# Performance work log

Hardware: AMD Instinct MI355X
Metric: run time of the kernel (lower is better)

## Reference

```python
import jax, jax.numpy as jnp
import numpy as np

PAD = 1
STRIDE = 1


def setup_inputs() -> dict:
    key = jax.random.key(0)
    kx, kw, kb = jax.random.split(key, 3)
    C_IN, C_OUT, K, H, W = 128, 256, 3, 256, 256
    lim = 1.0 / np.sqrt(C_IN * K * K)
    x = jax.random.normal(kx, (C_IN, H, W), dtype=jnp.float32)
    weight = jax.random.uniform(kw, (C_OUT, C_IN, K, K), minval=-lim, maxval=lim, dtype=jnp.float32)
    bias = jax.random.uniform(kb, (C_OUT, 1, 1), minval=-lim, maxval=lim, dtype=jnp.float32)
    return {"x": x, "weight": weight, "bias": bias}


def reference(x, weight, bias):
    # Original does per-channel jnp.pad then a scan-based im2col + einsum
    # 'oijk,ihwjk->ohw'. That is exactly a standard cross-correlation conv,
    # expressed here with the efficient fused primitive (same math).
    out = jax.lax.conv_general_dilated(
        x[None],                      # (1, c, h, w)
        weight,                       # (o, i, k, k)
        window_strides=(STRIDE, STRIDE),
        padding=[(PAD, PAD), (PAD, PAD)],
        dimension_numbers=("NCHW", "OIHW", "NCHW"),
    )[0]                              # (o, h', w')
    return out + bias
```

## Files before the change

### kernel.cpp

```cpp
#include <hip/hip_runtime.h>
#include <hip/hip_bf16.h>
#include <stdint.h>


#define CIN   128
#define COUT  256
#define HH    256
#define WW    256
#define HP    258
#define WP    258
#define XP_ELEMS (HP * WP * CIN)

typedef __attribute__((ext_vector_type(8))) __bf16 bf16x8;
typedef __attribute__((ext_vector_type(4))) float  floatx4;
typedef __attribute__((ext_vector_type(8))) short  short8;

__global__ void zero_border(unsigned short* __restrict__ xp) {
    int p  = blockIdx.x;
    int ch = threadIdx.x;
    int hp, wp;
    if (p < 258)      { hp = 0;   wp = p; }
    else if (p < 516) { hp = 257; wp = p - 258; }
    else { int s = p - 516; hp = 1 + (s >> 1); wp = (s & 1) * 257; }
    xp[(hp * WP + wp) * CIN + ch] = 0;
}

__global__ __launch_bounds__(256) void xpose_pad(const float* __restrict__ x,
                                                 unsigned short* __restrict__ xp) {
    __shared__ __align__(16) unsigned short tile[64][136];
    int h  = blockIdx.x;
    int w0 = blockIdx.y << 6;
    int t  = threadIdx.x;
    int wl  = t & 63;
    int icq = t >> 6;
    const float* src = x + h * WW + w0 + wl;
#pragma unroll
    for (int icb = 0; icb < 32; ++icb) {
        int ic = icb * 4 + icq;
        __hip_bfloat16 b = __float2bfloat16(src[ic * (HH * WW)]);
        tile[wl][ic] = __builtin_bit_cast(unsigned short, b);
    }
    __syncthreads();
    int wl2 = t >> 2, q = t & 3;
    const short8* s8 = (const short8*)&tile[wl2][q * 32];
    short8* d8 = (short8*)(xp + ((size_t)(h + 1) * WP + (w0 + 1) + wl2) * CIN + q * 32);
#pragma unroll
    for (int i = 0; i < 4; ++i) d8[i] = s8[i];
}

__global__ __launch_bounds__(256) void wpack(const float* __restrict__ w,
                                             unsigned short* __restrict__ wp) {
    int idx = blockIdx.x * 256 + threadIdx.x;
    int kk  = idx >> 15;
    int rem = idx & 32767;
    __hip_bfloat16 b = __float2bfloat16(w[rem * 9 + kk]);
    wp[idx] = __builtin_bit_cast(unsigned short, b);
}

__global__ __launch_bounds__(512, 2) void conv_mfma(
    const unsigned short* __restrict__ xp,
    const unsigned short* __restrict__ wpk,
    const float* __restrict__ bias,
    float* __restrict__ out) {
    __shared__ __align__(16) unsigned short x_lds[2 * 16384];

    const int tid  = threadIdx.x;
    const int lane = tid & 63;
    const int wv   = tid >> 6;
    const int l15  = lane & 15;
    const int lg   = lane >> 4;
    const int wave_m = (wv >> 2) << 7;
    const int wave_n = (wv & 3) << 6;

    const int orig = blockIdx.x;
    const int h    = ((orig & 7) << 5) | (orig >> 3);

    const int s0 = (tid & 255) * CIN + (tid >> 8) * 8;

    auto stage = [&](int buf, int kh, int kw, int kk, int icq) {
        unsigned short* base = x_lds + buf * 16384;
        const unsigned short* asrc = wpk + (size_t)kk * (COUT * CIN) + icq * 32 + s0;
        const unsigned short* bsrc = xp + ((size_t)(h + kh) * WP + kw) * CIN + icq * 32 + s0;
        __builtin_amdgcn_global_load_lds(
            (const __attribute__((address_space(1))) void*)asrc,
            (__attribute__((address_space(3))) void*)(base + tid * 8), 16, 0, 0);
        __builtin_amdgcn_global_load_lds(
            (const __attribute__((address_space(1))) void*)(asrc + 16),
            (__attribute__((address_space(3))) void*)(base + 4096 + tid * 8), 16, 0, 0);
        __builtin_amdgcn_global_load_lds(
            (const __attribute__((address_space(1))) void*)bsrc,
            (__attribute__((address_space(3))) void*)(base + 8192 + tid * 8), 16, 0, 0);
        __builtin_amdgcn_global_load_lds(
            (const __attribute__((address_space(1))) void*)(bsrc + 16),
            (__attribute__((address_space(3))) void*)(base + 12288 + tid * 8), 16, 0, 0);
    };

    floatx4 acc[8][4];
#pragma unroll
    for (int fi = 0; fi < 8; ++fi)
#pragma unroll
        for (int fj = 0; fj < 4; ++fj) {
            floatx4 z = {0.f, 0.f, 0.f, 0.f};
            acc[fi][fj] = z;
        }

    stage(0, 0, 0, 0, 0);
    __syncthreads();

#pragma unroll
    for (int kk = 0; kk < 9; ++kk) {
#pragma unroll
        for (int icq = 0; icq < 4; ++icq) {
            const int t   = kk * 4 + icq;
            const int cur = t & 1;

            if (t < 35) {
                const int tn  = t + 1;
                const int kkn = tn >> 2, icqn = tn & 3;
                const int khn = kkn / 3, kwn = kkn - khn * 3;
                stage(cur ^ 1, khn, kwn, kkn, icqn);
            }

            const unsigned short* Ab = x_lds + cur * 16384;
            const unsigned short* Bb = Ab + 8192;
            bf16x8 a[8], b[4];
#pragma unroll
            for (int fj = 0; fj < 4; ++fj)
                b[fj] = *(const bf16x8*)(Bb + (lg * 256 + wave_n + fj * 16 + l15) * 8);
#pragma unroll
            for (int fi = 0; fi < 8; ++fi)
                a[fi] = *(const bf16x8*)(Ab + (lg * 256 + wave_m + fi * 16 + l15) * 8);

            __builtin_amdgcn_s_setprio(1);
#pragma unroll
            for (int fi = 0; fi < 8; ++fi)
#pragma unroll
                for (int fj = 0; fj < 4; ++fj)
                    acc[fi][fj] = __builtin_amdgcn_mfma_f32_16x16x32_bf16(
                        a[fi], b[fj], acc[fi][fj], 0, 0, 0);
            __builtin_amdgcn_s_setprio(0);

            __syncthreads();
        }
    }

    const int nbase = h * WW + wave_n + l15;
#pragma unroll
    for (int fi = 0; fi < 8; ++fi) {
        int mrow = wave_m + fi * 16 + lg * 4;
#pragma unroll
        for (int r = 0; r < 4; ++r) {
            float bv = bias[mrow + r];
#pragma unroll
            for (int fj = 0; fj < 4; ++fj)
                out[(size_t)(mrow + r) * (HH * WW) + nbase + fj * 16] = acc[fi][fj][r] + bv;
        }
    }
}

extern "C" void kernel_launch(void* const* d_in, const int* in_sizes, int n_in,
                              void* d_out, int out_size, void* d_ws, size_t ws_size,
                              hipStream_t stream) {
    (void)in_sizes; (void)n_in; (void)out_size; (void)ws_size;
    const float* x    = (const float*)d_in[0];
    const float* w    = (const float*)d_in[1];
    const float* bias = (const float*)d_in[2];
    float* out = (float*)d_out;

    unsigned short* xp  = (unsigned short*)d_ws;
    unsigned short* wpk = xp + XP_ELEMS;

    zero_border<<<dim3(1028), dim3(128), 0, stream>>>(xp);
    xpose_pad<<<dim3(256, 4), dim3(256), 0, stream>>>(x, xp);
    wpack<<<dim3(1152), dim3(256), 0, stream>>>(w, wpk);
    conv_mfma<<<dim3(256), dim3(512), 0, stream>>>(xp, wpk, bias, out);
}
```

Before: 154.8 us.

## Merge prep kernels and double K-chunk per stage with XOR-swizzled LDS

Three preprocessing kernels (border zeroing, transpose-pad, weight pack) are merged into one launch, and the border zeroing now uses 16-byte stores. The conv kernel stages 64 input channels per step instead of 32, halving the number of barriers (18 stages instead of 36), and stores rows of 64 contiguous channels with an XOR swizzle to avoid LDS bank conflicts. LDS use doubles to 128 KB per block, which at two blocks per CU may exceed LDS capacity and reduce occupancy.

```diff
diff --git a/kernel.cpp b/kernel.cpp
--- a/kernel.cpp
+++ b/kernel.cpp
@@ -15,46 +15,51 @@
 typedef __attribute__((ext_vector_type(4))) float  floatx4;
 typedef __attribute__((ext_vector_type(8))) short  short8;
 
-__global__ void zero_border(unsigned short* __restrict__ xp) {
-    int p  = blockIdx.x;
-    int ch = threadIdx.x;
-    int hp, wp;
-    if (p < 258)      { hp = 0;   wp = p; }
-    else if (p < 516) { hp = 257; wp = p - 258; }
-    else { int s = p - 516; hp = 1 + (s >> 1); wp = (s & 1) * 257; }
-    xp[(hp * WP + wp) * CIN + ch] = 0;
-}
+#define AS1 __attribute__((address_space(1)))
+#define AS3 __attribute__((address_space(3)))
 
-__global__ __launch_bounds__(256) void xpose_pad(const float* __restrict__ x,
-                                                 unsigned short* __restrict__ xp) {
+__global__ __launch_bounds__(256) void prep(const float* __restrict__ x,
+                                            const float* __restrict__ w,
+                                            unsigned short* __restrict__ xp,
+                                            unsigned short* __restrict__ wpk) {
     __shared__ __align__(16) unsigned short tile[64][136];
-    int h  = blockIdx.x;
-    int w0 = blockIdx.y << 6;
-    int t  = threadIdx.x;
-    int wl  = t & 63;
-    int icq = t >> 6;
-    const float* src = x + h * WW + w0 + wl;
+    const int bid = blockIdx.x;
+    const int t   = threadIdx.x;
+    if (bid < 1024) {
+        int h  = bid >> 2;
+        int w0 = (bid & 3) << 6;
+        int wl = t & 63, icq = t >> 6;
+        const float* src = x + h * WW + w0 + wl;
 #pragma unroll
-    for (int icb = 0; icb < 32; ++icb) {
-        int ic = icb * 4 + icq;
-        __hip_bfloat16 b = __float2bfloat16(src[ic * (HH * WW)]);
-        tile[wl][ic] = __builtin_bit_cast(unsigned short, b);
+        for (int icb = 0; icb < 32; ++icb) {
+            int ic = icb * 4 + icq;
+            __hip_bfloat16 b = __float2bfloat16(src[ic * (HH * WW)]);
+            tile[wl][ic] = __builtin_bit_cast(unsigned short, b);
+        }
+        __syncthreads();
+        int wl2 = t >> 2, q = t & 3;
+        const short8* s8 = (const short8*)&tile[wl2][q * 32];
+        short8* d8 = (short8*)(xp + ((size_t)(h + 1) * WP + (w0 + 1) + wl2) * CIN + q * 32);
+#pragma unroll
+        for (int i = 0; i < 4; ++i) d8[i] = s8[i];
+    } else if (bid < 2176) {
+        int idx = (bid - 1024) * 256 + t;
+        int kk  = idx >> 15;
+        int rem = idx & 32767;
+        __hip_bfloat16 b = __float2bfloat16(w[rem * 9 + kk]);
+        wpk[idx] = __builtin_bit_cast(unsigned short, b);
+    } else {
+        int cid = (bid - 2176) * 256 + t;
+        if (cid < 16448) {
+            int p = cid >> 4, oct = cid & 15;
+            int hp, wp;
+            if (p < 258)      { hp = 0;   wp = p; }
+            else if (p < 516) { hp = 257; wp = p - 258; }
+            else { int s = p - 516; hp = 1 + (s >> 1); wp = (s & 1) * 257; }
+            short8 z = {0, 0, 0, 0, 0, 0, 0, 0};
+            *(short8*)(xp + ((size_t)hp * WP + wp) * CIN + oct * 8) = z;
+        }
     }
-    __syncthreads();
-    int wl2 = t >> 2, q = t & 3;
-    const short8* s8 = (const short8*)&tile[wl2][q * 32];
-    short8* d8 = (short8*)(xp + ((size_t)(h + 1) * WP + (w0 + 1) + wl2) * CIN + q * 32);
-#pragma unroll
-    for (int i = 0; i < 4; ++i) d8[i] = s8[i];
-}
-
-__global__ __launch_bounds__(256) void wpack(const float* __restrict__ w,
-                                             unsigned short* __restrict__ wp) {
-    int idx = blockIdx.x * 256 + threadIdx.x;
-    int kk  = idx >> 15;
-    int rem = idx & 32767;
-    __hip_bfloat16 b = __float2bfloat16(w[rem * 9 + kk]);
-    wp[idx] = __builtin_bit_cast(unsigned short, b);
 }
 
 __global__ __launch_bounds__(512, 2) void conv_mfma(
@@ -62,7 +67,7 @@
     const unsigned short* __restrict__ wpk,
     const float* __restrict__ bias,
     float* __restrict__ out) {
-    __shared__ __align__(16) unsigned short x_lds[2 * 16384];
+    __shared__ __align__(16) unsigned short x_lds[2 * 32768];
 
     const int tid  = threadIdx.x;
     const int lane = tid & 63;
@@ -75,24 +80,22 @@
     const int orig = blockIdx.x;
     const int h    = ((orig & 7) << 5) | (orig >> 3);
 
-    const int s0 = (tid & 255) * CIN + (tid >> 8) * 8;
+    const int soff = (tid >> 3) * CIN + ((((tid & 7) ^ ((tid >> 3) & 7))) << 3);
 
-    auto stage = [&](int buf, int kh, int kw, int kk, int icq) {
-        unsigned short* base = x_lds + buf * 16384;
-        const unsigned short* asrc = wpk + (size_t)kk * (COUT * CIN) + icq * 32 + s0;
-        const unsigned short* bsrc = xp + ((size_t)(h + kh) * WP + kw) * CIN + icq * 32 + s0;
-        __builtin_amdgcn_global_load_lds(
-            (const __attribute__((address_space(1))) void*)asrc,
-            (__attribute__((address_space(3))) void*)(base + tid * 8), 16, 0, 0);
-        __builtin_amdgcn_global_load_lds(
-            (const __attribute__((address_space(1))) void*)(asrc + 16),
-            (__attribute__((address_space(3))) void*)(base + 4096 + tid * 8), 16, 0, 0);
-        __builtin_amdgcn_global_load_lds(
-            (const __attribute__((address_space(1))) void*)bsrc,
-            (__attribute__((address_space(3))) void*)(base + 8192 + tid * 8), 16, 0, 0);
-        __builtin_amdgcn_global_load_lds(
-            (const __attribute__((address_space(1))) void*)(bsrc + 16),
-            (__attribute__((address_space(3))) void*)(base + 12288 + tid * 8), 16, 0, 0);
+    auto stage = [&](int buf, int kk, int kh, int kw, int hf) {
+        unsigned short* base = x_lds + buf * 32768;
+        const unsigned short* asrc = wpk + (size_t)kk * (COUT * CIN) + hf * 64 + soff;
+        const unsigned short* bsrc = xp + ((size_t)(h + kh) * WP + kw) * CIN + hf * 64 + soff;
+#pragma unroll
+        for (int i = 0; i < 4; ++i)
+            __builtin_amdgcn_global_load_lds(
+                (const AS1 void*)(asrc + i * 8192),
+                (AS3 void*)(base + i * 4096 + tid * 8), 16, 0, 0);
+#pragma unroll
+        for (int i = 0; i < 4; ++i)
+            __builtin_amdgcn_global_load_lds(
+                (const AS1 void*)(bsrc + i * 8192),
+                (AS3 void*)(base + 16384 + i * 4096 + tid * 8), 16, 0, 0);
     };
 
     floatx4 acc[8][4];
@@ -104,32 +107,35 @@
             acc[fi][fj] = z;
         }
 
+    const int aoct = (lg ^ (l15 & 7)) << 3;
+
     stage(0, 0, 0, 0, 0);
     __syncthreads();
 
 #pragma unroll
-    for (int kk = 0; kk < 9; ++kk) {
+    for (int t2 = 0; t2 < 18; ++t2) {
+        const int cur = t2 & 1;
+
+        if (t2 < 17) {
+            const int tn  = t2 + 1;
+            const int kkn = tn >> 1, hfn = tn & 1;
+            const int khn = kkn / 3, kwn = kkn - khn * 3;
+            stage(cur ^ 1, kkn, khn, kwn, hfn);
+        }
+
+        const unsigned short* Ab = x_lds + cur * 32768;
 #pragma unroll
-        for (int icq = 0; icq < 4; ++icq) {
-            const int t   = kk * 4 + icq;
-            const int cur = t & 1;
-
-            if (t < 35) {
-                const int tn  = t + 1;
-                const int kkn = tn >> 2, icqn = tn & 3;
-                const int khn = kkn / 3, kwn = kkn - khn * 3;
-                stage(cur ^ 1, khn, kwn, kkn, icqn);
-            }
-
-            const unsigned short* Ab = x_lds + cur * 16384;
-            const unsigned short* Bb = Ab + 8192;
+        for (int ks = 0; ks < 2; ++ks) {
+            const int kx = ks << 5;
             bf16x8 a[8], b[4];
 #pragma unroll
             for (int fj = 0; fj < 4; ++fj)
-                b[fj] = *(const bf16x8*)(Bb + (lg * 256 + wave_n + fj * 16 + l15) * 8);
+                b[fj] = *(const bf16x8*)(
+                    Ab + 16384 + ((wave_n + fj * 16 + l15) << 6) + (aoct ^ kx));
 #pragma unroll
             for (int fi = 0; fi < 8; ++fi)
-                a[fi] = *(const bf16x8*)(Ab + (lg * 256 + wave_m + fi * 16 + l15) * 8);
+                a[fi] = *(const bf16x8*)(
+                    Ab + ((wave_m + fi * 16 + l15) << 6) + (aoct ^ kx));
 
             __builtin_amdgcn_s_setprio(1);
 #pragma unroll
@@ -139,9 +145,9 @@
                     acc[fi][fj] = __builtin_amdgcn_mfma_f32_16x16x32_bf16(
                         a[fi], b[fj], acc[fi][fj], 0, 0, 0);
             __builtin_amdgcn_s_setprio(0);
+        }
 
-            __syncthreads();
-        }
+        __syncthreads();
     }
 
     const int nbase = h * WW + wave_n + l15;
@@ -170,8 +176,6 @@
     unsigned short* xp  = (unsigned short*)d_ws;
     unsigned short* wpk = xp + XP_ELEMS;
 
-    zero_border<<<dim3(1028), dim3(128), 0, stream>>>(xp);
-    xpose_pad<<<dim3(256, 4), dim3(256), 0, stream>>>(x, xp);
-    wpack<<<dim3(1152), dim3(256), 0, stream>>>(w, wpk);
+    prep<<<dim3(2241), dim3(256), 0, stream>>>(x, w, xp, wpk);
     conv_mfma<<<dim3(256), dim3(512), 0, stream>>>(xp, wpk, bias, out);
 }
```

Result: faster. 131.9 us (-14.8%).
